# Optimization experiments

Measured on AMD Instinct MI355X. Metric: run time of the kernel, lower is better.

Reference implementation:

```python
import jax, jax.numpy as jnp
import numpy as np
import math

N, E, D, H, L, DIN, NEP = 20000, 320000, 128, 8, 4, 16, 4
DFF = 4 * D
DH = D // H
SCALE = 1.0 / math.sqrt(DH)


def _ln(x, s, b, eps=1e-5):
    mu = x.mean(-1, keepdims=True)
    var = ((x - mu) ** 2).mean(-1, keepdims=True)
    return (x - mu) * jax.lax.rsqrt(var + eps) * s + b


def _attn(h, src, dst, ew, Wq, Wk, Wv, Wo, Wo_b):
    n = h.shape[0]
    Q = (h @ Wq).reshape(n, H, DH)
    K = (h @ Wk).reshape(n, H, DH)
    V = (h @ Wv).reshape(n, H, DH)
    # per-edge scores: [E, H]; ew is sigmoid(edge_feat.sum(-1, keepdims)) -> [E, 1]
    scores = (Q[src] * K[dst]).sum(-1) * SCALE * ew
    msg = V[dst] * scores[:, :, None]                       # [E, H, DH]
    sums = jax.ops.segment_sum(msg, dst, num_segments=n)    # [N, H, DH]
    cnt = jax.ops.segment_sum(jnp.ones((msg.shape[0],), h.dtype), dst, num_segments=n)
    out = sums / jnp.maximum(cnt, 1.0)[:, None, None]       # segment-mean (zeros if no edges)
    return out.reshape(n, D) @ Wo + Wo_b


def setup_inputs() -> dict:
    key = jax.random.key(0)
    ks = iter(jax.random.split(key, 40))
    rn = lambda *s: jax.random.normal(next(ks), s, jnp.float32) * 0.02
    inp = {
        'x': jax.random.normal(next(ks), (N, DIN), jnp.float32),
        'edge_index': jax.random.randint(next(ks), (2, E), 0, N),
        'edge_attr': jax.random.normal(next(ks), (E, 1), jnp.float32),
        'in_w': rn(DIN, D), 'in_b': jnp.zeros((D,)),
        'ee_w1': rn(1, D // 4), 'ee_b1': jnp.zeros((D // 4,)),
        'ee_w2': rn(D // 4, D // 2), 'ee_b2': jnp.zeros((D // 2,)),
        'Wq': rn(L, D, D), 'Wk': rn(L, D, D), 'Wv': rn(L, D, D),
        'Wo': rn(L, D, D), 'Wo_b': jnp.zeros((L, D)),
        'ff_w1': rn(L, D, DFF), 'ff_b1': jnp.zeros((L, DFF)),
        'ff_w2': rn(L, DFF, D), 'ff_b2': jnp.zeros((L, D)),
        'ln1_s': jnp.ones((L, D)), 'ln1_b': jnp.zeros((L, D)),
        'ln2_s': jnp.ones((L, D)), 'ln2_b': jnp.zeros((L, D)),
        'ec_w1': rn(D * 2 + D // 2, D), 'ec_b1': jnp.zeros((D,)),
        'ec_w2': rn(D, D // 2), 'ec_b2': jnp.zeros((D // 2,)),
        'ec_w3': rn(D // 2, 1), 'ec_b3': jnp.zeros((1,)),
        'pp_w1': rn(D * 2 + D // 2, D), 'pp_b1': jnp.zeros((D,)),
        'pp_w2': rn(D, D // 2), 'pp_b2': jnp.zeros((D // 2,)),
        'pp_w3': rn(D // 2, NEP), 'pp_b3': jnp.zeros((NEP,)),
    }
    return inp


def reference(x, edge_index, edge_attr, in_w, in_b, ee_w1, ee_b1, ee_w2, ee_b2,
              Wq, Wk, Wv, Wo, Wo_b, ff_w1, ff_b1, ff_w2, ff_b2,
              ln1_s, ln1_b, ln2_s, ln2_b,
              ec_w1, ec_b1, ec_w2, ec_b2, ec_w3, ec_b3,
              pp_w1, pp_b1, pp_w2, pp_b2, pp_w3, pp_b3):
    src, dst = edge_index[0], edge_index[1]
    h = x @ in_w + in_b                                     # [N, D]
    edge_feat = jax.nn.relu(edge_attr @ ee_w1 + ee_b1) @ ee_w2 + ee_b2  # [E, D/2]
    ew = jax.nn.sigmoid(edge_feat.sum(-1, keepdims=True))   # [E, 1]
    for l in range(L):
        a = _attn(h, src, dst, ew, Wq[l], Wk[l], Wv[l], Wo[l], Wo_b[l])
        h = _ln(h + a, ln1_s[l], ln1_b[l])
        f = jax.nn.relu(h @ ff_w1[l] + ff_b1[l]) @ ff_w2[l] + ff_b2[l]
        h = _ln(h + f, ln2_s[l], ln2_b[l])
    ef = jnp.concatenate([h[src], h[dst], edge_feat], axis=1)  # [E, 2.5*D]
    z = jax.nn.relu(ef @ ec_w1 + ec_b1)
    z = jax.nn.relu(z @ ec_w2 + ec_b2)
    edge_logits = (z @ ec_w3 + ec_b3).squeeze(-1)
    p = jax.nn.relu(ef @ pp_w1 + pp_b1)
    p = jax.nn.relu(p @ pp_w2 + pp_b2)
    edge_params = jax.nn.softplus(p @ pp_w3 + pp_b3) + 1e-6
    return edge_logits, edge_params
```

## Files before the change

### kernel.cpp

```cpp
#include <hip/hip_runtime.h>
#include <hip/hip_bf16.h>
#include <math.h>

#define N_NODES 20000
#define N_EDGES 320000
#define D 128
#define DFF 512
#define DIN 16
#define NLAYER 4
#define SCALE 0.25f
#define KE1 288

typedef __hip_bfloat16 bf16;
typedef __attribute__((ext_vector_type(8))) __bf16 bf16x8_t;
typedef __attribute__((ext_vector_type(4))) float f32x4;

__global__ void k_input_proj(const float* __restrict__ x, const float* __restrict__ in_w,
                             const float* __restrict__ in_b, float* __restrict__ h,
                             __bf16* __restrict__ h_bf) {
  int node = blockIdx.x;
  int j = threadIdx.x;
  __shared__ float xs[DIN];
  if (j < DIN) xs[j] = x[node * DIN + j];
  __syncthreads();
  float acc = in_b[j];
  for (int k = 0; k < DIN; ++k) acc = fmaf(xs[k], in_w[k * D + j], acc);
  h[(size_t)node * D + j] = acc;
  h_bf[(size_t)node * D + j] = (__bf16)acc;
}

__global__ void k_edge_prep(const float* __restrict__ ea, const float* __restrict__ w1,
                            const float* __restrict__ b1, const float* __restrict__ w2,
                            const float* __restrict__ b2, const int* __restrict__ dst,
                            float* __restrict__ ew, float* __restrict__ cnt) {
  __shared__ float rs[32], w1s[32], b1s[32];
  __shared__ float b2sum;
  int tid = threadIdx.x;
  if (tid < 32) {
    float s = 0.f;
    for (int j = 0; j < 64; ++j) s += w2[tid * 64 + j];
    rs[tid] = s;
    w1s[tid] = w1[tid];
    b1s[tid] = b1[tid];
  }
  if (tid == 0) {
    float s = 0.f;
    for (int j = 0; j < 64; ++j) s += b2[j];
    b2sum = s;
  }
  __syncthreads();
  int e = blockIdx.x * blockDim.x + tid;
  if (e >= N_EDGES) return;
  float a = ea[e];
  float s = b2sum;
  for (int i = 0; i < 32; ++i) {
    float t = fmaxf(fmaf(a, w1s[i], b1s[i]), 0.f);
    s = fmaf(t, rs[i], s);
  }
  ew[e] = 1.f / (1.f + expf(-s));
  atomicAdd(&cnt[dst[e]], 1.f);
}

__global__ void k_cvt_all(const float* __restrict__ Wq, const float* __restrict__ Wk,
                          const float* __restrict__ Wv, const float* __restrict__ ffw1,
                          const float* __restrict__ ffw2, const float* __restrict__ Wo,
                          const float* __restrict__ ecw2, const float* __restrict__ ppw2,
                          __bf16* __restrict__ wqkvT, __bf16* __restrict__ w1T,
                          __bf16* __restrict__ w2T, __bf16* __restrict__ woT,
                          __bf16* __restrict__ w2ET, __bf16* __restrict__ w2PT) {
  int t = blockIdx.x * 256 + threadIdx.x;
  if (t < 196608) {
    int l = t / 49152, u = t % 49152;
    int m = u / 16384, v = u % 16384;
    int n = v / 128, k = v % 128;
    const float* W = (m == 0) ? Wq : (m == 1) ? Wk : Wv;
    wqkvT[t] = (__bf16)W[l * 16384 + k * 128 + n];
  } else if (t < 196608 + 262144) {
    int u = t - 196608;
    int l = u / 65536, v = u % 65536;
    int n = v / 128, k = v % 128;
    w1T[u] = (__bf16)ffw1[l * 65536 + k * 512 + n];
  } else if (t < 458752 + 262144) {
    int u = t - 458752;
    int l = u / 65536, v = u % 65536;
    int n = v / 512, k = v % 512;
    w2T[u] = (__bf16)ffw2[l * 65536 + k * 128 + n];
  } else if (t < 720896 + 65536) {
    int u = t - 720896;
    int l = u / 16384, v = u % 16384;
    int n = v / 128, k = v % 128;
    woT[u] = (__bf16)Wo[l * 16384 + k * 128 + n];
  } else if (t < 786432 + 8192) {
    int u = t - 786432;
    int n = u / 128, k = u % 128;
    w2ET[u] = (__bf16)ecw2[k * 64 + n];
  } else if (t < 794624 + 8192) {
    int u = t - 794624;
    int n = u / 128, k = u % 128;
    w2PT[u] = (__bf16)ppw2[k * 64 + n];
  }
}

__global__ void k_prep(const float* __restrict__ ec_w1, const float* __restrict__ ec_b1,
                       const float* __restrict__ pp_w1, const float* __restrict__ pp_b1,
                       const float* __restrict__ ee_w2, const float* __restrict__ ee_b2,
                       __bf16* __restrict__ w1ET, __bf16* __restrict__ w1PT,
                       float* __restrict__ b1Ep, float* __restrict__ b1Pp) {
  int tid = threadIdx.x;
  int p = tid >> 7, n = tid & 127;
  const float* w1 = p ? pp_w1 : ec_w1;
  const float* bb = p ? pp_b1 : ec_b1;
  __bf16* wT = p ? w1PT : w1ET;
  float* bo = p ? b1Pp : b1Ep;
  for (int k = 0; k < 256; ++k) wT[n * KE1 + k] = (__bf16)w1[k * 128 + n];
  for (int i = 0; i < 32; ++i) {
    float m = 0.f;
    for (int j = 0; j < 64; ++j) m = fmaf(ee_w2[i * 64 + j], w1[(256 + j) * 128 + n], m);
    wT[n * KE1 + 256 + i] = (__bf16)m;
  }
  float b = bb[n];
  for (int j = 0; j < 64; ++j) b = fmaf(ee_b2[j], w1[(256 + j) * 128 + n], b);
  bo[n] = b;
}

__global__ __launch_bounds__(256) void k_qkv(const __bf16* __restrict__ h_bf,
                                             const __bf16* __restrict__ wT,
                                             __bf16* __restrict__ Q, __bf16* __restrict__ K,
                                             __bf16* __restrict__ V) {
  int tid = threadIdx.x, wv = tid >> 6, lane = tid & 63;
  int lr = lane & 15, lk = (lane >> 4) * 8, g4 = (lane >> 4) * 4;
  int n0 = blockIdx.x * 16;
  const __bf16* hp = h_bf + (size_t)(n0 + lr) * D;
  f32x4 acc[6];
#pragma unroll
  for (int j = 0; j < 6; ++j) acc[j] = (f32x4){0.f, 0.f, 0.f, 0.f};
#pragma unroll
  for (int ks = 0; ks < 4; ++ks) {
    bf16x8_t aF = *(const bf16x8_t*)&hp[ks * 32 + lk];
#pragma unroll
    for (int j = 0; j < 6; ++j) {
      int nb = wv * 6 + j;
      bf16x8_t bF = *(const bf16x8_t*)&wT[(nb * 16 + lr) * 128 + ks * 32 + lk];
      acc[j] = __builtin_amdgcn_mfma_f32_16x16x32_bf16(aF, bF, acc[j], 0, 0, 0);
    }
  }
#pragma unroll
  for (int j = 0; j < 6; ++j) {
    int nb = wv * 6 + j;
    int m = nb >> 3;
    __bf16* out = (m == 0) ? Q : (m == 1) ? K : V;
#pragma unroll
    for (int r = 0; r < 4; ++r)
      out[(size_t)(n0 + g4 + r) * D + (nb & 7) * 16 + lr] = (__bf16)acc[j][r];
  }
}

__global__ void k_edge_attn(const int* __restrict__ src, const int* __restrict__ dst,
                            const float* __restrict__ ew, const __bf16* __restrict__ Q,
                            const __bf16* __restrict__ K, float* __restrict__ sc) {
  int t = blockIdx.x * blockDim.x + threadIdx.x;
  if (t >= N_EDGES * 8) return;
  int e = t >> 3, hd = t & 7;
  int s = src[e], d = dst[e];
  const __bf16* q = Q + (size_t)s * D + hd * 16;
  const __bf16* k = K + (size_t)d * D + hd * 16;
  bf16x8_t q0 = *(const bf16x8_t*)q, q1 = *(const bf16x8_t*)(q + 8);
  bf16x8_t k0 = *(const bf16x8_t*)k, k1 = *(const bf16x8_t*)(k + 8);
  float p = 0.f;
#pragma unroll
  for (int i = 0; i < 8; ++i) p = fmaf((float)q0[i], (float)k0[i], p);
#pragma unroll
  for (int i = 0; i < 8; ++i) p = fmaf((float)q1[i], (float)k1[i], p);
  atomicAdd(&sc[d * 8 + hd], p * SCALE * ew[e]);
}

__global__ __launch_bounds__(256) void k_node(
    float* __restrict__ sc, const float* __restrict__ cnt, const __bf16* __restrict__ Vin,
    float* __restrict__ h, __bf16* __restrict__ h_bf, const __bf16* __restrict__ woT,
    const float* __restrict__ Wo_b, const float* __restrict__ ln1_s,
    const float* __restrict__ ln1_b, const __bf16* __restrict__ w1T,
    const __bf16* __restrict__ w2T, const float* __restrict__ b1,
    const float* __restrict__ b2, const float* __restrict__ ln2_s,
    const float* __restrict__ ln2_b, const __bf16* __restrict__ wqkvT_next,
    __bf16* __restrict__ Q, __bf16* __restrict__ K, __bf16* __restrict__ Vout,
    const __bf16* __restrict__ w1ET, const __bf16* __restrict__ w1PT,
    __bf16* __restrict__ PsE, __bf16* __restrict__ PdE, __bf16* __restrict__ PsP,
    __bf16* __restrict__ PdP) {
  __shared__ __bf16 z0[16][136];
  __shared__ __bf16 z1[16][520];
  __shared__ float lnb[4][16][2];
  int tid = threadIdx.x, wv = tid >> 6, lane = tid & 63;
  int lr = lane & 15, lk = (lane >> 4) * 8, g4 = (lane >> 4) * 4;
  int n0 = blockIdx.x * 16;
  int nd = n0 + lr;

  float inv = 1.f / fmaxf(cnt[nd], 1.f);
  float scs[8];
#pragma unroll
  for (int i = 0; i < 8; ++i) scs[i] = sc[nd * 8 + i] * inv;
  f32x4 acc[2];
#pragma unroll
  for (int j = 0; j < 2; ++j) {
    float bv = Wo_b[(wv * 2 + j) * 16 + lr];
    acc[j] = (f32x4){bv, bv, bv, bv};
  }
#pragma unroll
  for (int ks = 0; ks < 4; ++ks) {
    bf16x8_t v8 = *(const bf16x8_t*)&Vin[(size_t)nd * D + ks * 32 + lk];
    float m = scs[(ks * 32 + lk) >> 4];
    bf16x8_t aF;
#pragma unroll
    for (int i = 0; i < 8; ++i) aF[i] = (__bf16)((float)v8[i] * m);
#pragma unroll
    for (int j = 0; j < 2; ++j) {
      bf16x8_t bF = *(const bf16x8_t*)&woT[((wv * 2 + j) * 16 + lr) * 128 + ks * 32 + lk];
      acc[j] = __builtin_amdgcn_mfma_f32_16x16x32_bf16(aF, bF, acc[j], 0, 0, 0);
    }
  }
  float y[2][4];
#pragma unroll
  for (int j = 0; j < 2; ++j)
#pragma unroll
    for (int r = 0; r < 4; ++r)
      y[j][r] = h[(size_t)(n0 + g4 + r) * D + (wv * 2 + j) * 16 + lr] + acc[j][r];
  float s_[4], q_[4];
#pragma unroll
  for (int r = 0; r < 4; ++r) {
    float a0 = y[0][r], a1 = y[1][r];
    float s = a0 + a1, q = fmaf(a0, a0, a1 * a1);
    s += __shfl_xor(s, 1); s += __shfl_xor(s, 2); s += __shfl_xor(s, 4); s += __shfl_xor(s, 8);
    q += __shfl_xor(q, 1); q += __shfl_xor(q, 2); q += __shfl_xor(q, 4); q += __shfl_xor(q, 8);
    s_[r] = s; q_[r] = q;
  }
  if (lr == 0) {
#pragma unroll
    for (int r = 0; r < 4; ++r) {
      lnb[wv][g4 + r][0] = s_[r];
      lnb[wv][g4 + r][1] = q_[r];
    }
  }
  __syncthreads();
  if (tid < 128) sc[n0 * 8 + tid] = 0.f;
  float mean[4], rstd[4];
#pragma unroll
  for (int r = 0; r < 4; ++r) {
    float sm = 0.f, sq = 0.f;
#pragma unroll
    for (int w2i = 0; w2i < 4; ++w2i) {
      sm += lnb[w2i][g4 + r][0];
      sq += lnb[w2i][g4 + r][1];
    }
    float mu = sm * (1.f / 128.f);
    mean[r] = mu;
    rstd[r] = rsqrtf(sq * (1.f / 128.f) - mu * mu + 1e-5f);
  }
#pragma unroll
  for (int j = 0; j < 2; ++j) {
    int col = (wv * 2 + j) * 16 + lr;
    float lsv = ln1_s[col], lbv = ln1_b[col];
#pragma unroll
    for (int r = 0; r < 4; ++r) {
      y[j][r] = (y[j][r] - mean[r]) * rstd[r] * lsv + lbv;
      z0[g4 + r][col] = (__bf16)y[j][r];
    }
  }
  __syncthreads();

  f32x4 a1[8];
#pragma unroll
  for (int j = 0; j < 8; ++j) {
    float bv = b1[(wv * 8 + j) * 16 + lr];
    a1[j] = (f32x4){bv, bv, bv, bv};
  }
#pragma unroll
  for (int ks = 0; ks < 4; ++ks) {
    bf16x8_t aF = *(const bf16x8_t*)&z0[lr][ks * 32 + lk];
#pragma unroll
    for (int j = 0; j < 8; ++j) {
      bf16x8_t bF = *(const bf16x8_t*)&w1T[((wv * 8 + j) * 16 + lr) * 128 + ks * 32 + lk];
      a1[j] = __builtin_amdgcn_mfma_f32_16x16x32_bf16(aF, bF, a1[j], 0, 0, 0);
    }
  }
#pragma unroll
  for (int j = 0; j < 8; ++j)
#pragma unroll
    for (int r = 0; r < 4; ++r)
      z1[g4 + r][(wv * 8 + j) * 16 + lr] = (__bf16)fmaxf(a1[j][r], 0.f);
  __syncthreads();

  f32x4 a2[2];
#pragma unroll
  for (int j = 0; j < 2; ++j) {
    float bv = b2[(wv * 2 + j) * 16 + lr];
    a2[j] = (f32x4){bv, bv, bv, bv};
  }
#pragma unroll
  for (int ks = 0; ks < 16; ++ks) {
    bf16x8_t aF = *(const bf16x8_t*)&z1[lr][ks * 32 + lk];
#pragma unroll
    for (int j = 0; j < 2; ++j) {
      bf16x8_t bF = *(const bf16x8_t*)&w2T[((wv * 2 + j) * 16 + lr) * 512 + ks * 32 + lk];
      a2[j] = __builtin_amdgcn_mfma_f32_16x16x32_bf16(aF, bF, a2[j], 0, 0, 0);
    }
  }
#pragma unroll
  for (int j = 0; j < 2; ++j)
#pragma unroll
    for (int r = 0; r < 4; ++r) y[j][r] += a2[j][r];
#pragma unroll
  for (int r = 0; r < 4; ++r) {
    float a0 = y[0][r], a1v = y[1][r];
    float s = a0 + a1v, q = fmaf(a0, a0, a1v * a1v);
    s += __shfl_xor(s, 1); s += __shfl_xor(s, 2); s += __shfl_xor(s, 4); s += __shfl_xor(s, 8);
    q += __shfl_xor(q, 1); q += __shfl_xor(q, 2); q += __shfl_xor(q, 4); q += __shfl_xor(q, 8);
    s_[r] = s; q_[r] = q;
  }
  if (lr == 0) {
#pragma unroll
    for (int r = 0; r < 4; ++r) {
      lnb[wv][g4 + r][0] = s_[r];
      lnb[wv][g4 + r][1] = q_[r];
    }
  }
  __syncthreads();
#pragma unroll
  for (int r = 0; r < 4; ++r) {
    float sm = 0.f, sq = 0.f;
#pragma unroll
    for (int w2i = 0; w2i < 4; ++w2i) {
      sm += lnb[w2i][g4 + r][0];
      sq += lnb[w2i][g4 + r][1];
    }
    float mu = sm * (1.f / 128.f);
    mean[r] = mu;
    rstd[r] = rsqrtf(sq * (1.f / 128.f) - mu * mu + 1e-5f);
  }
#pragma unroll
  for (int j = 0; j < 2; ++j) {
    int col = (wv * 2 + j) * 16 + lr;
    float lsv = ln2_s[col], lbv = ln2_b[col];
#pragma unroll
    for (int r = 0; r < 4; ++r) {
      float yv = (y[j][r] - mean[r]) * rstd[r] * lsv + lbv;
      y[j][r] = yv;
      h[(size_t)(n0 + g4 + r) * D + col] = yv;
      h_bf[(size_t)(n0 + g4 + r) * D + col] = (__bf16)yv;
    }
  }

#pragma unroll
  for (int j = 0; j < 2; ++j)
#pragma unroll
    for (int r = 0; r < 4; ++r)
      z0[g4 + r][(wv * 2 + j) * 16 + lr] = (__bf16)y[j][r];
  __syncthreads();

  if (wqkvT_next) {
    f32x4 aq[6];
#pragma unroll
    for (int j = 0; j < 6; ++j) aq[j] = (f32x4){0.f, 0.f, 0.f, 0.f};
#pragma unroll
    for (int ks = 0; ks < 4; ++ks) {
      bf16x8_t aF = *(const bf16x8_t*)&z0[lr][ks * 32 + lk];
#pragma unroll
      for (int j = 0; j < 6; ++j) {
        int nb = wv * 6 + j;
        bf16x8_t bF = *(const bf16x8_t*)&wqkvT_next[(nb * 16 + lr) * 128 + ks * 32 + lk];
        aq[j] = __builtin_amdgcn_mfma_f32_16x16x32_bf16(aF, bF, aq[j], 0, 0, 0);
      }
    }
#pragma unroll
    for (int j = 0; j < 6; ++j) {
      int nb = wv * 6 + j;
      int m = nb >> 3;
      __bf16* out = (m == 0) ? Q : (m == 1) ? K : Vout;
#pragma unroll
      for (int r = 0; r < 4; ++r)
        out[(size_t)(n0 + g4 + r) * D + (nb & 7) * 16 + lr] = (__bf16)aq[j][r];
    }
  } else {
    const __bf16* wsrc = (wv & 2) ? w1PT : w1ET;
    int koff = (wv & 1) ? 128 : 0;
    __bf16* outP = (wv == 0) ? PsE : (wv == 1) ? PdE : (wv == 2) ? PsP : PdP;
    f32x4 ap[8];
#pragma unroll
    for (int nb = 0; nb < 8; ++nb) ap[nb] = (f32x4){0.f, 0.f, 0.f, 0.f};
#pragma unroll
    for (int ks = 0; ks < 4; ++ks) {
      bf16x8_t aF = *(const bf16x8_t*)&z0[lr][ks * 32 + lk];
#pragma unroll
      for (int nb = 0; nb < 8; ++nb) {
        bf16x8_t bF = *(const bf16x8_t*)&wsrc[(nb * 16 + lr) * KE1 + koff + ks * 32 + lk];
        ap[nb] = __builtin_amdgcn_mfma_f32_16x16x32_bf16(aF, bF, ap[nb], 0, 0, 0);
      }
    }
#pragma unroll
    for (int nb = 0; nb < 8; ++nb)
#pragma unroll
      for (int r = 0; r < 4; ++r)
        outP[(size_t)(n0 + g4 + r) * D + nb * 16 + lr] = (__bf16)ap[nb][r];
  }
}

__global__ __launch_bounds__(256) void k_final(
    const int* __restrict__ src, const int* __restrict__ dst, const float* __restrict__ ea,
    const float* __restrict__ ee_w1, const float* __restrict__ ee_b1,
    const __bf16* __restrict__ w1ET, const __bf16* __restrict__ w1PT,
    const __bf16* __restrict__ w2ET, const __bf16* __restrict__ w2PT,
    const float* __restrict__ b1Ep, const float* __restrict__ b1Pp,
    const __bf16* __restrict__ PsE, const __bf16* __restrict__ PdE,
    const __bf16* __restrict__ PsP, const __bf16* __restrict__ PdP,
    const float* __restrict__ ec_b2, const float* __restrict__ ec_w3,
    const float* __restrict__ ec_b3, const float* __restrict__ pp_b2,
    const float* __restrict__ pp_w3, const float* __restrict__ pp_b3,
    float* __restrict__ out_logits, float* __restrict__ out_params) {
  __shared__ __bf16 z1[2][32][136];
  int tid = threadIdx.x, wv = tid >> 6, lane = tid & 63;
  int lr = lane & 15, lk = (lane >> 4) * 8, g4 = (lane >> 4) * 4;
  int p = wv & 1, m0 = (wv >> 1) * 16;
  int e0 = blockIdx.x * 32;
  int e = e0 + m0 + lr;
  float av = ea[e];
  bf16x8_t aR;
#pragma unroll
  for (int i = 0; i < 8; ++i)
    aR[i] = (__bf16)fmaxf(fmaf(av, ee_w1[lk + i], ee_b1[lk + i]), 0.f);

  const __bf16* w1x = p ? w1PT : w1ET;
  const float* b1x = p ? b1Pp : b1Ep;
  const __bf16* w2x = p ? w2PT : w2ET;
  const float* b2x = p ? pp_b2 : ec_b2;

  f32x4 acc[8];
#pragma unroll
  for (int nb = 0; nb < 8; ++nb) {
    float bv = b1x[nb * 16 + lr];
    acc[nb] = (f32x4){bv, bv, bv, bv};
  }
#pragma unroll
  for (int nb = 0; nb < 8; ++nb) {
    bf16x8_t bF = *(const bf16x8_t*)&w1x[(nb * 16 + lr) * KE1 + 256 + lk];
    acc[nb] = __builtin_amdgcn_mfma_f32_16x16x32_bf16(aR, bF, acc[nb], 0, 0, 0);
  }
#pragma unroll
  for (int nb = 0; nb < 8; ++nb)
#pragma unroll
    for (int r = 0; r < 4; ++r) z1[p][m0 + g4 + r][nb * 16 + lr] = (__bf16)acc[nb][r];

  {
    int em = lane >> 2, c4 = lane & 3;
    int ee = e0 + m0 + em;
    const __bf16* Ps = p ? PsP : PsE;
    const __bf16* Pd = p ? PdP : PdE;
    const __bf16* psrow = Ps + (size_t)src[ee] * D + c4 * 32;
    const __bf16* pdrow = Pd + (size_t)dst[ee] * D + c4 * 32;
#pragma unroll
    for (int ch = 0; ch < 4; ++ch) {
      bf16x8_t a = *(const bf16x8_t*)&psrow[ch * 8];
      bf16x8_t b = *(const bf16x8_t*)&pdrow[ch * 8];
      bf16x8_t f = *(const bf16x8_t*)&z1[p][m0 + em][c4 * 32 + ch * 8];
      bf16x8_t o;
#pragma unroll
      for (int i = 0; i < 8; ++i)
        o[i] = (__bf16)fmaxf((float)a[i] + (float)b[i] + (float)f[i], 0.f);
      *(bf16x8_t*)&z1[p][m0 + em][c4 * 32 + ch * 8] = o;
    }
  }

  f32x4 acc2[4];
#pragma unroll
  for (int nb = 0; nb < 4; ++nb) {
    float bv = b2x[nb * 16 + lr];
    acc2[nb] = (f32x4){bv, bv, bv, bv};
  }
#pragma unroll
  for (int ks = 0; ks < 4; ++ks) {
    bf16x8_t aF = *(const bf16x8_t*)&z1[p][m0 + lr][ks * 32 + lk];
#pragma unroll
    for (int nb = 0; nb < 4; ++nb) {
      bf16x8_t bF = *(const bf16x8_t*)&w2x[(nb * 16 + lr) * 128 + ks * 32 + lk];
      acc2[nb] = __builtin_amdgcn_mfma_f32_16x16x32_bf16(aF, bF, acc2[nb], 0, 0, 0);
    }
  }

  if (p == 0) {
    float w3v[4];
#pragma unroll
    for (int nb = 0; nb < 4; ++nb) w3v[nb] = ec_w3[nb * 16 + lr];
    float b3 = ec_b3[0];
#pragma unroll
    for (int r = 0; r < 4; ++r) {
      float s = 0.f;
#pragma unroll
      for (int nb = 0; nb < 4; ++nb) s = fmaf(fmaxf(acc2[nb][r], 0.f), w3v[nb], s);
      s += __shfl_xor(s, 1);
      s += __shfl_xor(s, 2);
      s += __shfl_xor(s, 4);
      s += __shfl_xor(s, 8);
      if (lr == 0) out_logits[e0 + m0 + g4 + r] = s + b3;
    }
  } else {
    float wp[4][4];
#pragma unroll
    for (int nb = 0; nb < 4; ++nb)
#pragma unroll
      for (int c = 0; c < 4; ++c) wp[nb][c] = pp_w3[(nb * 16 + lr) * 4 + c];
#pragma unroll
    for (int c = 0; c < 4; ++c) {
      float b3 = pp_b3[c];
#pragma unroll
      for (int r = 0; r < 4; ++r) {
        float s = 0.f;
#pragma unroll
        for (int nb = 0; nb < 4; ++nb) s = fmaf(fmaxf(acc2[nb][r], 0.f), wp[nb][c], s);
        s += __shfl_xor(s, 1);
        s += __shfl_xor(s, 2);
        s += __shfl_xor(s, 4);
        s += __shfl_xor(s, 8);
        if (lr == 0) {
          float xx = s + b3;
          float sp = fmaxf(xx, 0.f) + log1pf(expf(-fabsf(xx)));
          out_params[(size_t)(e0 + m0 + g4 + r) * 4 + c] = sp + 1e-6f;
        }
      }
    }
  }
}

extern "C" void kernel_launch(void* const* d_in, const int* in_sizes, int n_in,
                              void* d_out, int out_size, void* d_ws, size_t ws_size,
                              hipStream_t stream) {
  const float* x = (const float*)d_in[0];
  const int* eidx = (const int*)d_in[1];
  const float* eattr = (const float*)d_in[2];
  const float* in_w = (const float*)d_in[3];
  const float* in_b = (const float*)d_in[4];
  const float* ee_w1 = (const float*)d_in[5];
  const float* ee_b1 = (const float*)d_in[6];
  const float* ee_w2 = (const float*)d_in[7];
  const float* ee_b2 = (const float*)d_in[8];
  const float* Wq = (const float*)d_in[9];
  const float* Wk = (const float*)d_in[10];
  const float* Wv = (const float*)d_in[11];
  const float* Wo = (const float*)d_in[12];
  const float* Wo_b = (const float*)d_in[13];
  const float* ff_w1 = (const float*)d_in[14];
  const float* ff_b1 = (const float*)d_in[15];
  const float* ff_w2 = (const float*)d_in[16];
  const float* ff_b2 = (const float*)d_in[17];
  const float* ln1_s = (const float*)d_in[18];
  const float* ln1_b = (const float*)d_in[19];
  const float* ln2_s = (const float*)d_in[20];
  const float* ln2_b = (const float*)d_in[21];
  const float* ec_w1 = (const float*)d_in[22];
  const float* ec_b1 = (const float*)d_in[23];
  const float* ec_w2 = (const float*)d_in[24];
  const float* ec_b2 = (const float*)d_in[25];
  const float* ec_w3 = (const float*)d_in[26];
  const float* ec_b3 = (const float*)d_in[27];
  const float* pp_w1 = (const float*)d_in[28];
  const float* pp_b1 = (const float*)d_in[29];
  const float* pp_w2 = (const float*)d_in[30];
  const float* pp_b2 = (const float*)d_in[31];
  const float* pp_w3 = (const float*)d_in[32];
  const float* pp_b3 = (const float*)d_in[33];

  const int* src = eidx;
  const int* dst = eidx + N_EDGES;

  char* wsb = (char*)d_ws;
  float* sc = (float*)wsb;
  float* cnt = (float*)(wsb + 640000);
  float* h = (float*)(wsb + 720000);
  __bf16* h_bf = (__bf16*)(wsb + 10960000);
  __bf16* Q = (__bf16*)(wsb + 16080000);
  __bf16* Kb = (__bf16*)(wsb + 21200000);
  __bf16* V0 = (__bf16*)(wsb + 26320000);
  __bf16* V1 = (__bf16*)(wsb + 31440000);
  float* ew = (float*)(wsb + 36560000);
  __bf16* wqkvT = (__bf16*)(wsb + 37840000);
  __bf16* w1T = (__bf16*)(wsb + 38233216);
  __bf16* w2T = (__bf16*)(wsb + 38757504);
  __bf16* woT = (__bf16*)(wsb + 39281792);
  __bf16* w1ET = (__bf16*)(wsb + 39412864);
  __bf16* w1PT = (__bf16*)(wsb + 39486592);
  __bf16* w2ET = (__bf16*)(wsb + 39560320);
  __bf16* w2PT = (__bf16*)(wsb + 39576704);
  float* b1Ep = (float*)(wsb + 39593088);
  float* b1Pp = (float*)(wsb + 39593600);

  hipMemsetAsync(cnt, 0, N_NODES * sizeof(float), stream);
  hipMemsetAsync(sc, 0, N_NODES * 8 * sizeof(float), stream);
  k_input_proj<<<N_NODES, D, 0, stream>>>(x, in_w, in_b, h, h_bf);
  k_edge_prep<<<(N_EDGES + 255) / 256, 256, 0, stream>>>(eattr, ee_w1, ee_b1, ee_w2, ee_b2,
                                                         dst, ew, cnt);
  k_cvt_all<<<(802816 + 255) / 256, 256, 0, stream>>>(Wq, Wk, Wv, ff_w1, ff_w2, Wo, ec_w2,
                                                      pp_w2, wqkvT, w1T, w2T, woT, w2ET, w2PT);
  k_prep<<<1, 256, 0, stream>>>(ec_w1, ec_b1, pp_w1, pp_b1, ee_w2, ee_b2, w1ET, w1PT, b1Ep,
                                b1Pp);

  __bf16* PsE = Q;
  __bf16* PdE = Kb;
  __bf16* PsP = V0;
  __bf16* PdP = V1;

  int nblk = N_NODES / 16;
  k_qkv<<<nblk, 256, 0, stream>>>(h_bf, wqkvT, Q, Kb, V0);
  for (int l = 0; l < NLAYER; ++l) {
    __bf16* Vin = (l & 1) ? V1 : V0;
    __bf16* Vout = (l & 1) ? V0 : V1;
    k_edge_attn<<<(N_EDGES * 8 + 255) / 256, 256, 0, stream>>>(src, dst, ew, Q, Kb, sc);
    k_node<<<nblk, 256, 0, stream>>>(
        sc, cnt, Vin, h, h_bf, woT + (size_t)l * 16384, Wo_b + l * D, ln1_s + l * D,
        ln1_b + l * D, w1T + (size_t)l * 65536, w2T + (size_t)l * 65536, ff_b1 + l * DFF,
        ff_b2 + l * D, ln2_s + l * D, ln2_b + l * D,
        (l < NLAYER - 1) ? (wqkvT + (size_t)(l + 1) * 49152) : (const __bf16*)nullptr, Q, Kb,
        Vout, w1ET, w1PT, PsE, PdE, PsP, PdP);
  }

  float* out_logits = (float*)d_out;
  float* out_params = out_logits + N_EDGES;
  k_final<<<N_EDGES / 32, 256, 0, stream>>>(src, dst, eattr, ee_w1, ee_b1, w1ET, w1PT, w2ET,
                                            w2PT, b1Ep, b1Pp, PsE, PdE, PsP, PdP, ec_b2,
                                            ec_w3, ec_b3, pp_b2, pp_w3, pp_b3, out_logits,
                                            out_params);
}
```

Before: 601.1 us.

## Store Q/K head-major and map edge-attention blocks per head

Q and K are now written head-major ([H][N][16]), and the score accumulator is laid out head-major as well. Each edge-attention block handles one head for 256 edges, so the random gathers for a head stay inside a 640KB slice that is more likely to stay cache-resident. The cost is that src, dst and ew are each read eight times (once per head), and the row-major Q/K stores from the MFMA tiles become more scattered.

```diff
diff --git a/kernel.cpp b/kernel.cpp
--- a/kernel.cpp
+++ b/kernel.cpp
@@ -10,6 +10,7 @@
 #define NLAYER 4
 #define SCALE 0.25f
 #define KE1 288
+#define N16 (N_NODES * 16)
 
 typedef __hip_bfloat16 bf16;
 typedef __attribute__((ext_vector_type(8))) __bf16 bf16x8_t;
@@ -125,7 +126,7 @@
 
 __global__ __launch_bounds__(256) void k_qkv(const __bf16* __restrict__ h_bf,
                                              const __bf16* __restrict__ wT,
-                                             __bf16* __restrict__ Q, __bf16* __restrict__ K,
+                                             __bf16* __restrict__ Qh, __bf16* __restrict__ Kh,
                                              __bf16* __restrict__ V) {
   int tid = threadIdx.x, wv = tid >> 6, lane = tid & 63;
   int lr = lane & 15, lk = (lane >> 4) * 8, g4 = (lane >> 4) * 4;
@@ -148,22 +149,28 @@
   for (int j = 0; j < 6; ++j) {
     int nb = wv * 6 + j;
     int m = nb >> 3;
-    __bf16* out = (m == 0) ? Q : (m == 1) ? K : V;
-#pragma unroll
-    for (int r = 0; r < 4; ++r)
-      out[(size_t)(n0 + g4 + r) * D + (nb & 7) * 16 + lr] = (__bf16)acc[j][r];
+    if (m == 2) {
+#pragma unroll
+      for (int r = 0; r < 4; ++r)
+        V[(size_t)(n0 + g4 + r) * D + (nb & 7) * 16 + lr] = (__bf16)acc[j][r];
+    } else {
+      __bf16* out = (m == 0) ? Qh : Kh;
+#pragma unroll
+      for (int r = 0; r < 4; ++r)
+        out[(size_t)(nb & 7) * N16 + (size_t)(n0 + g4 + r) * 16 + lr] = (__bf16)acc[j][r];
+    }
   }
 }
 
 __global__ void k_edge_attn(const int* __restrict__ src, const int* __restrict__ dst,
-                            const float* __restrict__ ew, const __bf16* __restrict__ Q,
-                            const __bf16* __restrict__ K, float* __restrict__ sc) {
-  int t = blockIdx.x * blockDim.x + threadIdx.x;
-  if (t >= N_EDGES * 8) return;
-  int e = t >> 3, hd = t & 7;
+                            const float* __restrict__ ew, const __bf16* __restrict__ Qh,
+                            const __bf16* __restrict__ Kh, float* __restrict__ sc) {
+  int bid = blockIdx.x;
+  int h = bid / 1250;
+  int e = (bid - h * 1250) * 256 + threadIdx.x;
   int s = src[e], d = dst[e];
-  const __bf16* q = Q + (size_t)s * D + hd * 16;
-  const __bf16* k = K + (size_t)d * D + hd * 16;
+  const __bf16* q = Qh + (size_t)h * N16 + (size_t)s * 16;
+  const __bf16* k = Kh + (size_t)h * N16 + (size_t)d * 16;
   bf16x8_t q0 = *(const bf16x8_t*)q, q1 = *(const bf16x8_t*)(q + 8);
   bf16x8_t k0 = *(const bf16x8_t*)k, k1 = *(const bf16x8_t*)(k + 8);
   float p = 0.f;
@@ -171,7 +178,7 @@
   for (int i = 0; i < 8; ++i) p = fmaf((float)q0[i], (float)k0[i], p);
 #pragma unroll
   for (int i = 0; i < 8; ++i) p = fmaf((float)q1[i], (float)k1[i], p);
-  atomicAdd(&sc[d * 8 + hd], p * SCALE * ew[e]);
+  atomicAdd(&sc[h * N_NODES + d], p * SCALE * ew[e]);
 }
 
 __global__ __launch_bounds__(256) void k_node(
@@ -182,7 +189,7 @@
     const __bf16* __restrict__ w2T, const float* __restrict__ b1,
     const float* __restrict__ b2, const float* __restrict__ ln2_s,
     const float* __restrict__ ln2_b, const __bf16* __restrict__ wqkvT_next,
-    __bf16* __restrict__ Q, __bf16* __restrict__ K, __bf16* __restrict__ Vout,
+    __bf16* __restrict__ Qh, __bf16* __restrict__ Kh, __bf16* __restrict__ Vout,
     const __bf16* __restrict__ w1ET, const __bf16* __restrict__ w1PT,
     __bf16* __restrict__ PsE, __bf16* __restrict__ PdE, __bf16* __restrict__ PsP,
     __bf16* __restrict__ PdP) {
@@ -197,7 +204,7 @@
   float inv = 1.f / fmaxf(cnt[nd], 1.f);
   float scs[8];
 #pragma unroll
-  for (int i = 0; i < 8; ++i) scs[i] = sc[nd * 8 + i] * inv;
+  for (int i = 0; i < 8; ++i) scs[i] = sc[i * N_NODES + nd] * inv;
   f32x4 acc[2];
 #pragma unroll
   for (int j = 0; j < 2; ++j) {
@@ -240,7 +247,7 @@
     }
   }
   __syncthreads();
-  if (tid < 128) sc[n0 * 8 + tid] = 0.f;
+  if (tid < 128) sc[(tid >> 4) * N_NODES + n0 + (tid & 15)] = 0.f;
   float mean[4], rstd[4];
 #pragma unroll
   for (int r = 0; r < 4; ++r) {
@@ -373,10 +380,16 @@
     for (int j = 0; j < 6; ++j) {
       int nb = wv * 6 + j;
       int m = nb >> 3;
-      __bf16* out = (m == 0) ? Q : (m == 1) ? K : Vout;
-#pragma unroll
-      for (int r = 0; r < 4; ++r)
-        out[(size_t)(n0 + g4 + r) * D + (nb & 7) * 16 + lr] = (__bf16)aq[j][r];
+      if (m == 2) {
+#pragma unroll
+        for (int r = 0; r < 4; ++r)
+          Vout[(size_t)(n0 + g4 + r) * D + (nb & 7) * 16 + lr] = (__bf16)aq[j][r];
+      } else {
+        __bf16* out = (m == 0) ? Qh : Kh;
+#pragma unroll
+        for (int r = 0; r < 4; ++r)
+          out[(size_t)(nb & 7) * N16 + (size_t)(n0 + g4 + r) * 16 + lr] = (__bf16)aq[j][r];
+      }
     }
   } else {
     const __bf16* wsrc = (wv & 2) ? w1PT : w1ET;
@@ -609,7 +622,7 @@
   for (int l = 0; l < NLAYER; ++l) {
     __bf16* Vin = (l & 1) ? V1 : V0;
     __bf16* Vout = (l & 1) ? V0 : V1;
-    k_edge_attn<<<(N_EDGES * 8 + 255) / 256, 256, 0, stream>>>(src, dst, ew, Q, Kb, sc);
+    k_edge_attn<<<1250 * 8, 256, 0, stream>>>(src, dst, ew, Q, Kb, sc);
     k_node<<<nblk, 256, 0, stream>>>(
         sc, cnt, Vin, h, h_bf, woT + (size_t)l * 16384, Wo_b + l * D, ln1_s + l * D,
         ln1_b + l * D, w1T + (size_t)l * 65536, w2T + (size_t)l * 65536, ff_b1 + l * DFF,
```

Measured after the change: 1.111 ms. +84.9%, slower.
